# Optimization experiments

Hardware: AMD Instinct MI355X
Metric: run time of the kernel (lower is better)

Reference implementation:

```python
import jax, jax.numpy as jnp
import numpy as np

MARGIN = 0.3


def setup_inputs() -> dict:
    key = jax.random.key(0)
    k1, k2 = jax.random.split(key)
    inputs = jax.random.normal(k1, (8192, 128), dtype=jnp.float32)
    targets = jax.random.randint(k2, (8192,), 0, 512, dtype=jnp.int64)
    return {"inputs": inputs, "targets": targets}


def reference(inputs, targets):
    # inputs: [n, d], targets: [n]
    sq = jnp.sum(inputs * inputs, axis=1)  # [n]
    # dist[i,j] = ||x_i||^2 + ||x_j||^2 - 2 x_i . x_j
    dist = sq[:, None] + sq[None, :] - 2.0 * (inputs @ inputs.T)
    dist = jnp.sqrt(jnp.clip(dist, 1e-12, None))  # [n, n]
    mask = targets[:, None] == targets[None, :]  # True where same label
    # batch-hard mining: hardest positive (max) and hardest negative (min) per row.
    # Diagonal is always True, so every row has at least one positive.
    dist_ap = jnp.max(jnp.where(mask, dist, -jnp.inf), axis=1)  # [n]
    dist_an = jnp.min(jnp.where(mask, jnp.inf, dist), axis=1)  # [n]
    # MarginRankingLoss with y=1: mean(max(0, margin - (dist_an - dist_ap)))
    loss = jnp.mean(jnp.maximum(0.0, MARGIN - (dist_an - dist_ap)))
    prec = jnp.mean((dist_an > dist_ap).astype(jnp.float32))
    return loss, prec
```

## Files before the change

### kernel.cpp

```cpp
#include <hip/hip_runtime.h>
#include <hip/hip_bf16.h>
#include <math.h>

#define N 8192
#define D 128
#define MARGIN 0.3f

#define NSTRIP 64
#define BPS 11
#define TPB 6
#define GRID_MAIN (NSTRIP * BPS)

typedef float f32x4 __attribute__((ext_vector_type(4)));
typedef short bf16x8 __attribute__((ext_vector_type(8)));
typedef unsigned short u16x8 __attribute__((ext_vector_type(8)));

#define AS1 __attribute__((address_space(1)))
#define AS3 __attribute__((address_space(3)))

__device__ inline void gload_lds16(const void* g, void* l) {
    __builtin_amdgcn_global_load_lds((AS1 void*)(void*)(g), (AS3 void*)(l), 16, 0, 0);
}

__device__ inline unsigned short f2bf(float f) {
    unsigned u = __float_as_uint(f);
    unsigned r = (u + 0x7FFFu + ((u >> 16) & 1u)) >> 16;
    return (unsigned short)r;
}

__global__ __launch_bounds__(256) void convert_kernel(const float* __restrict__ X,
                                                      unsigned short* __restrict__ Xb,
                                                      float* __restrict__ sq,
                                                      unsigned* __restrict__ ap2,
                                                      unsigned* __restrict__ an2) {
    int tid = threadIdx.x;
    int row = blockIdx.x * 16 + (tid >> 4);
    int l = tid & 15;
    const float4* p = reinterpret_cast<const float4*>(X + (size_t)row * D + l * 8);
    float4 u = p[0];
    float4 v = p[1];
    float s = u.x*u.x + u.y*u.y + u.z*u.z + u.w*u.w
            + v.x*v.x + v.y*v.y + v.z*v.z + v.w*v.w;
    u16x8 o;
    o[0] = f2bf(u.x); o[1] = f2bf(u.y); o[2] = f2bf(u.z); o[3] = f2bf(u.w);
    o[4] = f2bf(v.x); o[5] = f2bf(v.y); o[6] = f2bf(v.z); o[7] = f2bf(v.w);
    *reinterpret_cast<u16x8*>(Xb + (size_t)row * D + l * 8) = o;
    #pragma unroll
    for (int off = 8; off >= 1; off >>= 1) s += __shfl_xor(s, off);
    if (l == 0) {
        sq[row] = s;
        ap2[row] = 0u;
        an2[row] = 0x7F7F7F7Fu;
    }
}

__global__ __launch_bounds__(256, 3) void triplet_main(
        const unsigned short* __restrict__ Xb,
        const int* __restrict__ lbl,
        const float* __restrict__ sq,
        unsigned* __restrict__ ap2,
        unsigned* __restrict__ an2) {
    __shared__ unsigned short As[128 * D];
    __shared__ unsigned short Bs[64 * D];

    const int bi = blockIdx.x / BPS;
    const int s  = blockIdx.x - bi * BPS;
    const int base = s * TPB;
    const int jwin0 = 2 * bi;

    const int tid = threadIdx.x;
    const int w = tid >> 6;
    const int lane = tid & 63;
    const int wr = w >> 1;
    const int wc = w & 1;
    const int quad = lane >> 4;
    const int lx = lane & 15;
    const int i0 = bi * 128;

    int lbl_i[16];
    float sqi_r[16];
    #pragma unroll
    for (int tr = 0; tr < 4; ++tr)
        #pragma unroll
        for (int v = 0; v < 4; ++v) {
            int row = i0 + wr * 64 + tr * 16 + quad * 4 + v;
            lbl_i[tr * 4 + v] = lbl[row];
            sqi_r[tr * 4 + v] = sq[row];
        }

    float m_ap[16], m_an[16];
    #pragma unroll
    for (int q = 0; q < 16; ++q) { m_ap[q] = -INFINITY; m_an[q] = INFINITY; }

    #pragma unroll
    for (int t = 0; t < 8; ++t) {
        int rbase = w * 32 + t * 4;
        int r = rbase + quad;
        int gc = lx ^ (r & 7);
        gload_lds16(Xb + (size_t)(i0 + r) * D + gc * 8, &As[rbase * D]);
    }
    {
        int jj0 = (jwin0 + base) & 127;
        #pragma unroll
        for (int t = 0; t < 4; ++t) {
            int rbase = w * 16 + t * 4;
            int r = rbase + quad;
            int gc = lx ^ (r & 7);
            gload_lds16(Xb + (size_t)(jj0 * 64 + r) * D + gc * 8, &Bs[rbase * D]);
        }
    }
    __syncthreads();

    #pragma unroll 1
    for (int t = 0; t < TPB; ++t) {
        const int o = base + t;
        const int jj = (jwin0 + o) & 127;

        float sqj[2]; int lblj[2];
        #pragma unroll
        for (int tc = 0; tc < 2; ++tc) {
            int jc = jj * 64 + wc * 32 + tc * 16 + lx;
            sqj[tc] = sq[jc];
            lblj[tc] = lbl[jc];
        }

        f32x4 acc[4][2];
        #pragma unroll
        for (int a = 0; a < 4; ++a)
            #pragma unroll
            for (int c = 0; c < 2; ++c)
                acc[a][c] = (f32x4){0.f, 0.f, 0.f, 0.f};

        #pragma unroll
        for (int ks = 0; ks < 4; ++ks) {
            bf16x8 af[4], bf[2];
            #pragma unroll
            for (int tr = 0; tr < 4; ++tr) {
                int rA = wr * 64 + tr * 16 + lx;
                int sc = (ks * 4 + quad) ^ (lx & 7);
                af[tr] = *reinterpret_cast<const bf16x8*>(&As[rA * D + sc * 8]);
            }
            #pragma unroll
            for (int tc = 0; tc < 2; ++tc) {
                int rB = wc * 32 + tc * 16 + lx;
                int sc = (ks * 4 + quad) ^ (lx & 7);
                bf[tc] = *reinterpret_cast<const bf16x8*>(&Bs[rB * D + sc * 8]);
            }
            #pragma unroll
            for (int tr = 0; tr < 4; ++tr)
                #pragma unroll
                for (int tc = 0; tc < 2; ++tc)
                    acc[tr][tc] = __builtin_amdgcn_mfma_f32_16x16x32_bf16(
                        af[tr], bf[tc], acc[tr][tc], 0, 0, 0);
        }

        __syncthreads();

        if (t + 1 < TPB) {
            int jjn = (jwin0 + o + 1) & 127;
            #pragma unroll
            for (int tt = 0; tt < 4; ++tt) {
                int rbase = w * 16 + tt * 4;
                int r = rbase + quad;
                int gc = lx ^ (r & 7);
                gload_lds16(Xb + (size_t)(jjn * 64 + r) * D + gc * 8, &Bs[rbase * D]);
            }
        }

        const bool jmine = (o >= 2) & (o < 64);
        #pragma unroll
        for (int tc = 0; tc < 2; ++tc) {
            float mApJ = -INFINITY, mAnJ = INFINITY;
            #pragma unroll
            for (int tr = 0; tr < 4; ++tr) {
                #pragma unroll
                for (int v = 0; v < 4; ++v) {
                    int q = tr * 4 + v;
                    float dot2 = -2.f * acc[tr][tc][v];
                    float vi = sqj[tc] + dot2;
                    float vj = sqi_r[q] + dot2;
                    bool same = (lblj[tc] == lbl_i[q]);
                    m_ap[q] = same ? fmaxf(m_ap[q], vi) : m_ap[q];
                    m_an[q] = same ? m_an[q] : fminf(m_an[q], vi);
                    mApJ = same ? fmaxf(mApJ, vj) : mApJ;
                    mAnJ = same ? mAnJ : fminf(mAnJ, vj);
                }
            }
            if (jmine) {
                #pragma unroll
                for (int off = 16; off <= 32; off <<= 1) {
                    mApJ = fmaxf(mApJ, __shfl_xor(mApJ, off));
                    mAnJ = fminf(mAnJ, __shfl_xor(mAnJ, off));
                }
                if (quad == 0) {
                    int jc = jj * 64 + wc * 32 + tc * 16 + lx;
                    float vap = fmaxf(sqj[tc] + mApJ, 1e-12f);
                    float van = fmaxf(sqj[tc] + mAnJ, 1e-12f);
                    atomicMax(&ap2[jc], __float_as_uint(vap));
                    atomicMin(&an2[jc], __float_as_uint(van));
                }
            }
        }

        if (t + 1 < TPB) __syncthreads();
    }

    #pragma unroll
    for (int off = 8; off >= 1; off >>= 1) {
        #pragma unroll
        for (int q = 0; q < 16; ++q) {
            m_ap[q] = fmaxf(m_ap[q], __shfl_xor(m_ap[q], off));
            m_an[q] = fminf(m_an[q], __shfl_xor(m_an[q], off));
        }
    }
    if (lx == 0) {
        #pragma unroll
        for (int tr = 0; tr < 4; ++tr) {
            #pragma unroll
            for (int v = 0; v < 4; ++v) {
                int q = tr * 4 + v;
                int row = i0 + wr * 64 + tr * 16 + quad * 4 + v;
                float vap = fmaxf(sqi_r[q] + m_ap[q], 1e-12f);
                float van = fmaxf(sqi_r[q] + m_an[q], 1e-12f);
                atomicMax(&ap2[row], __float_as_uint(vap));
                atomicMin(&an2[row], __float_as_uint(van));
            }
        }
    }
}

__global__ __launch_bounds__(1024) void finalize_kernel(const unsigned* __restrict__ ap2,
                                                        const unsigned* __restrict__ an2,
                                                        float* __restrict__ out) {
    int tid = threadIdx.x;
    float ls = 0.f, ps = 0.f;
    for (int row = tid; row < N; row += 1024) {
        float ap = sqrtf(__uint_as_float(ap2[row]));
        float an = sqrtf(__uint_as_float(an2[row]));
        ls += fmaxf(0.f, MARGIN - (an - ap));
        ps += (an > ap) ? 1.f : 0.f;
    }
    #pragma unroll
    for (int off = 32; off >= 1; off >>= 1) {
        ls += __shfl_xor(ls, off);
        ps += __shfl_xor(ps, off);
    }
    __shared__ float red[2][16];
    int w = tid >> 6;
    if ((tid & 63) == 0) { red[0][w] = ls; red[1][w] = ps; }
    __syncthreads();
    if (tid == 0) {
        float L = 0.f, P = 0.f;
        #pragma unroll
        for (int i = 0; i < 16; ++i) { L += red[0][i]; P += red[1][i]; }
        out[0] = L / (float)N;
        out[1] = P / (float)N;
    }
}

extern "C" void kernel_launch(void* const* d_in, const int* in_sizes, int n_in,
                              void* d_out, int out_size, void* d_ws, size_t ws_size,
                              hipStream_t stream) {
    const float* X = (const float*)d_in[0];
    const int* lbl = (const int*)d_in[1];
    float* out = (float*)d_out;

    float* sq = (float*)d_ws;
    unsigned* ap2 = (unsigned*)d_ws + N;
    unsigned* an2 = (unsigned*)d_ws + 2 * N;
    unsigned short* Xb = (unsigned short*)((char*)d_ws + 3 * N * sizeof(unsigned));

    convert_kernel<<<N / 16, 256, 0, stream>>>(X, Xb, sq, ap2, an2);
    triplet_main<<<GRID_MAIN, 256, 0, stream>>>(Xb, lbl, sq, ap2, an2);
    finalize_kernel<<<1, 1024, 0, stream>>>(ap2, an2, out);
}
```

Measured before the change: 92.98 us.

## Drop symmetric tile mining, keep A in registers, double-buffer B tiles

```diff
diff --git a/kernel.cpp b/kernel.cpp
--- a/kernel.cpp
+++ b/kernel.cpp
@@ -7,9 +7,8 @@
 #define MARGIN 0.3f
 
 #define NSTRIP 64
-#define BPS 11
-#define TPB 6
-#define GRID_MAIN (NSTRIP * BPS)
+#define CPS 12
+#define GRID_MAIN (NSTRIP * CPS)
 
 typedef float f32x4 __attribute__((ext_vector_type(4)));
 typedef short bf16x8 __attribute__((ext_vector_type(8)));
@@ -60,13 +59,14 @@
         const float* __restrict__ sq,
         unsigned* __restrict__ ap2,
         unsigned* __restrict__ an2) {
-    __shared__ unsigned short As[128 * D];
-    __shared__ unsigned short Bs[64 * D];
-
-    const int bi = blockIdx.x / BPS;
-    const int s  = blockIdx.x - bi * BPS;
-    const int base = s * TPB;
-    const int jwin0 = 2 * bi;
+    __shared__ unsigned short Bs[2][64 * D];
+    unsigned short* BsL = &Bs[0][0];
+
+    const int bi = blockIdx.x / CPS;
+    const int c  = blockIdx.x - bi * CPS;
+    const int jt0 = c * 10 + (c < 8 ? c : 8);
+    const int cnt = 10 + (c < 8 ? 1 : 0);
+    const int i0 = bi * 128;
 
     const int tid = threadIdx.x;
     const int w = tid >> 6;
@@ -75,46 +75,57 @@
     const int wc = w & 1;
     const int quad = lane >> 4;
     const int lx = lane & 15;
-    const int i0 = bi * 128;
-
-    int lbl_i[16];
-    float sqi_r[16];
-    #pragma unroll
-    for (int tr = 0; tr < 4; ++tr)
-        #pragma unroll
-        for (int v = 0; v < 4; ++v) {
-            int row = i0 + wr * 64 + tr * 16 + quad * 4 + v;
-            lbl_i[tr * 4 + v] = lbl[row];
-            sqi_r[tr * 4 + v] = sq[row];
-        }
-
-    float m_ap[16], m_an[16];
-    #pragma unroll
-    for (int q = 0; q < 16; ++q) { m_ap[q] = -INFINITY; m_an[q] = INFINITY; }
 
     #pragma unroll
     for (int t = 0; t < 8; ++t) {
         int rbase = w * 32 + t * 4;
         int r = rbase + quad;
         int gc = lx ^ (r & 7);
-        gload_lds16(Xb + (size_t)(i0 + r) * D + gc * 8, &As[rbase * D]);
-    }
+        gload_lds16(Xb + (size_t)(i0 + r) * D + gc * 8, BsL + rbase * D);
+    }
+
+    int lbl_i[16];
+    #pragma unroll
+    for (int tr = 0; tr < 4; ++tr)
+        #pragma unroll
+        for (int v = 0; v < 4; ++v)
+            lbl_i[tr * 4 + v] = lbl[i0 + wr * 64 + tr * 16 + quad * 4 + v];
+
+    __syncthreads();
+
+    bf16x8 af_r[4][4];
+    #pragma unroll
+    for (int tr = 0; tr < 4; ++tr) {
+        int rA = wr * 64 + tr * 16 + lx;
+        #pragma unroll
+        for (int ks = 0; ks < 4; ++ks) {
+            int sc = (ks * 4 + quad) ^ (lx & 7);
+            af_r[tr][ks] = *reinterpret_cast<const bf16x8*>(&BsL[rA * D + sc * 8]);
+        }
+    }
+    __syncthreads();
+
     {
-        int jj0 = (jwin0 + base) & 127;
+        int jj0 = jt0;
         #pragma unroll
         for (int t = 0; t < 4; ++t) {
             int rbase = w * 16 + t * 4;
             int r = rbase + quad;
             int gc = lx ^ (r & 7);
-            gload_lds16(Xb + (size_t)(jj0 * 64 + r) * D + gc * 8, &Bs[rbase * D]);
-        }
-    }
-    __syncthreads();
-
-    #pragma unroll 1
-    for (int t = 0; t < TPB; ++t) {
-        const int o = base + t;
-        const int jj = (jwin0 + o) & 127;
+            gload_lds16(Xb + (size_t)(jj0 * 64 + r) * D + gc * 8, BsL + rbase * D);
+        }
+    }
+
+    float m_ap[16], m_an[16];
+    #pragma unroll
+    for (int q = 0; q < 16; ++q) { m_ap[q] = -INFINITY; m_an[q] = INFINITY; }
+
+    __syncthreads();
+
+    for (int tt = 0; tt < cnt; ++tt) {
+        const int jj = jt0 + tt;
+        const int cur = tt & 1;
+        const unsigned short* curB = BsL + cur * (64 * D);
 
         float sqj[2]; int lblj[2];
         #pragma unroll
@@ -124,85 +135,58 @@
             lblj[tc] = lbl[jc];
         }
 
+        if (tt + 1 < cnt) {
+            unsigned short* nb = BsL + (cur ^ 1) * (64 * D);
+            int jn = jj + 1;
+            #pragma unroll
+            for (int t = 0; t < 4; ++t) {
+                int rbase = w * 16 + t * 4;
+                int r = rbase + quad;
+                int gc = lx ^ (r & 7);
+                gload_lds16(Xb + (size_t)(jn * 64 + r) * D + gc * 8, nb + rbase * D);
+            }
+        }
+
         f32x4 acc[4][2];
         #pragma unroll
         for (int a = 0; a < 4; ++a)
             #pragma unroll
-            for (int c = 0; c < 2; ++c)
-                acc[a][c] = (f32x4){0.f, 0.f, 0.f, 0.f};
+            for (int cc = 0; cc < 2; ++cc)
+                acc[a][cc] = (f32x4){0.f, 0.f, 0.f, 0.f};
 
         #pragma unroll
         for (int ks = 0; ks < 4; ++ks) {
-            bf16x8 af[4], bf[2];
-            #pragma unroll
-            for (int tr = 0; tr < 4; ++tr) {
-                int rA = wr * 64 + tr * 16 + lx;
-                int sc = (ks * 4 + quad) ^ (lx & 7);
-                af[tr] = *reinterpret_cast<const bf16x8*>(&As[rA * D + sc * 8]);
-            }
+            bf16x8 bf[2];
             #pragma unroll
             for (int tc = 0; tc < 2; ++tc) {
                 int rB = wc * 32 + tc * 16 + lx;
                 int sc = (ks * 4 + quad) ^ (lx & 7);
-                bf[tc] = *reinterpret_cast<const bf16x8*>(&Bs[rB * D + sc * 8]);
+                bf[tc] = *reinterpret_cast<const bf16x8*>(&curB[rB * D + sc * 8]);
             }
             #pragma unroll
             for (int tr = 0; tr < 4; ++tr)
                 #pragma unroll
                 for (int tc = 0; tc < 2; ++tc)
                     acc[tr][tc] = __builtin_amdgcn_mfma_f32_16x16x32_bf16(
-                        af[tr], bf[tc], acc[tr][tc], 0, 0, 0);
-        }
-
-        __syncthreads();
-
-        if (t + 1 < TPB) {
-            int jjn = (jwin0 + o + 1) & 127;
-            #pragma unroll
-            for (int tt = 0; tt < 4; ++tt) {
-                int rbase = w * 16 + tt * 4;
-                int r = rbase + quad;
-                int gc = lx ^ (r & 7);
-                gload_lds16(Xb + (size_t)(jjn * 64 + r) * D + gc * 8, &Bs[rbase * D]);
-            }
-        }
-
-        const bool jmine = (o >= 2) & (o < 64);
+                        af_r[tr][ks], bf[tc], acc[tr][tc], 0, 0, 0);
+        }
+
         #pragma unroll
         for (int tc = 0; tc < 2; ++tc) {
-            float mApJ = -INFINITY, mAnJ = INFINITY;
             #pragma unroll
             for (int tr = 0; tr < 4; ++tr) {
                 #pragma unroll
                 for (int v = 0; v < 4; ++v) {
                     int q = tr * 4 + v;
-                    float dot2 = -2.f * acc[tr][tc][v];
-                    float vi = sqj[tc] + dot2;
-                    float vj = sqi_r[q] + dot2;
+                    float vi = fmaf(-2.f, acc[tr][tc][v], sqj[tc]);
                     bool same = (lblj[tc] == lbl_i[q]);
                     m_ap[q] = same ? fmaxf(m_ap[q], vi) : m_ap[q];
                     m_an[q] = same ? m_an[q] : fminf(m_an[q], vi);
-                    mApJ = same ? fmaxf(mApJ, vj) : mApJ;
-                    mAnJ = same ? mAnJ : fminf(mAnJ, vj);
                 }
             }
-            if (jmine) {
-                #pragma unroll
-                for (int off = 16; off <= 32; off <<= 1) {
-                    mApJ = fmaxf(mApJ, __shfl_xor(mApJ, off));
-                    mAnJ = fminf(mAnJ, __shfl_xor(mAnJ, off));
-                }
-                if (quad == 0) {
-                    int jc = jj * 64 + wc * 32 + tc * 16 + lx;
-                    float vap = fmaxf(sqj[tc] + mApJ, 1e-12f);
-                    float van = fmaxf(sqj[tc] + mAnJ, 1e-12f);
-                    atomicMax(&ap2[jc], __float_as_uint(vap));
-                    atomicMin(&an2[jc], __float_as_uint(van));
-                }
-            }
-        }
-
-        if (t + 1 < TPB) __syncthreads();
+        }
+
+        if (tt + 1 < cnt) __syncthreads();
     }
 
     #pragma unroll
@@ -220,8 +204,9 @@
             for (int v = 0; v < 4; ++v) {
                 int q = tr * 4 + v;
                 int row = i0 + wr * 64 + tr * 16 + quad * 4 + v;
-                float vap = fmaxf(sqi_r[q] + m_ap[q], 1e-12f);
-                float van = fmaxf(sqi_r[q] + m_an[q], 1e-12f);
+                float sqi = sq[row];
+                float vap = fmaxf(sqi + m_ap[q], 1e-12f);
+                float van = fmaxf(sqi + m_an[q], 1e-12f);
                 atomicMax(&ap2[row], __float_as_uint(vap));
                 atomicMin(&an2[row], __float_as_uint(van));
             }
```

Result: slower. 104.8 us (+12.7%).
